# Kernel tuning notes

Hardware: AMD Instinct MI355X
Metric: run time of the kernel (lower is better)

Reference implementation:

```python
import jax, jax.numpy as jnp
import numpy as np
from jax import lax

# Dims from LSTMTagger class constants
B, S, LP = 1024, 128, 14       # sentences, words/sentence, padded chars/word
K, CE, WE, Lf = 3, 6, 10, 4    # char window, char emb, word emb, cnn filters
H, V, A, T = 6, 50000, 100, 135  # lstm hidden, vocab, alphabet, tagset
D = WE + Lf                     # lstm input dim = 14
LW = LP - K + 1                 # conv windows per word = 12


def setup_inputs() -> dict:
    key = jax.random.key(0)
    ks = jax.random.split(key, 14)
    n = lambda k, shp: jax.random.normal(k, shp, dtype=jnp.float32) * 0.1
    inp = {
        "word_idx": jax.random.randint(ks[0], (B, S), 0, V, dtype=jnp.int32),
        "char_idx": jax.random.randint(ks[1], (B, S, LP), 0, A, dtype=jnp.int32),
        "word_emb": n(ks[2], (V, WE)),
        "char_emb": n(ks[3], (A, CE)),
        "Wc": n(ks[4], (Lf, K * CE)),   # Conv1d(1, l, K*CE) weight, squeezed
        "bc": n(ks[5], (Lf,)),
        "Wih_f": n(ks[6], (4 * H, D)),
        "Whh_f": n(ks[7], (4 * H, H)),
        "b_f": n(ks[8], (4 * H,)),      # b_ih + b_hh fused (equivalent)
        "Wih_b": n(ks[9], (4 * H, D)),
        "Whh_b": n(ks[10], (4 * H, H)),
        "b_b": n(ks[11], (4 * H,)),
        "Wt": n(ks[12], (T, 2 * H)),
        "bt": n(ks[13], (T,)),
    }
    return inp


def _lstm_scan(xs, Wih, Whh, b):
    # xs: [S, B, D] -> hs: [S, B, H]; torch gate order i, f, g, o
    h0 = jnp.zeros((xs.shape[1], H), xs.dtype)

    def step(carry, xt):
        h, c = carry
        g = xt @ Wih.T + h @ Whh.T + b
        i, f, gg, o = jnp.split(g, 4, axis=-1)
        c = jax.nn.sigmoid(f) * c + jax.nn.sigmoid(i) * jnp.tanh(gg)
        h = jax.nn.sigmoid(o) * jnp.tanh(c)
        return (h, c), h

    _, hs = lax.scan(step, (h0, h0), xs)
    return hs


def reference(word_emb, char_emb, Wc, bc, Wih_f, Whh_f, b_f,
              Wih_b, Whh_b, b_b, Wt, bt, word_idx, char_idx):
    # per-word char CNN: sliding K-char windows, flatten, linear, max-pool
    ce = char_emb[char_idx]                              # [B,S,LP,CE]
    windows = jnp.concatenate([ce[:, :, i:i + LW] for i in range(K)], axis=-1)  # [B,S,LW,K*CE]
    phi = jnp.einsum('bswk,lk->bswl', windows, Wc) + bc  # [B,S,LW,Lf]
    char_repr = phi.max(axis=2)                          # [B,S,Lf]

    we = word_emb[word_idx]                              # [B,S,WE]
    x = jnp.concatenate([we, char_repr], axis=-1)        # [B,S,D]

    xs = x.transpose(1, 0, 2)                            # [S,B,D]
    hf = _lstm_scan(xs, Wih_f, Whh_f, b_f)               # forward direction
    hb = _lstm_scan(xs[::-1], Wih_b, Whh_b, b_b)[::-1]   # backward direction
    out = jnp.concatenate([hf, hb], axis=-1).transpose(1, 0, 2)  # [B,S,2H]

    tag_space = out @ Wt.T + bt                          # [B,S,T]
    return jax.nn.log_softmax(tag_space, axis=-1)
```

## Files before the change

### kernel.cpp

```cpp
#include <hip/hip_runtime.h>

#define B_   1024
#define S_   128
#define LP_  14
#define K_   3
#define CE_  6
#define WE_  10
#define LF_  4
#define H_   6
#define D_   14
#define T_   135
#define LW_  12
#define V_   50000
#define A_   100
#define NSEQ (B_ * 2)

static __device__ __forceinline__ float fsigm(float x) {
    return __frcp_rn(1.0f + __expf(-x));
}
static __device__ __forceinline__ float ftanh(float x) {
    return fmaf(2.0f, __frcp_rn(1.0f + __expf(-2.0f * x)), -1.0f);
}

static __device__ __forceinline__ float wave_sum64(float s) {
    int v = __float_as_int(s);
    float f;
    f = __int_as_float(__builtin_amdgcn_update_dpp(0, v, 0xB1, 0xF, 0xF, true));  s += f; v = __float_as_int(s);
    f = __int_as_float(__builtin_amdgcn_update_dpp(0, v, 0x4E, 0xF, 0xF, true));  s += f; v = __float_as_int(s);
    f = __int_as_float(__builtin_amdgcn_update_dpp(0, v, 0x141, 0xF, 0xF, true)); s += f; v = __float_as_int(s);
    f = __int_as_float(__builtin_amdgcn_update_dpp(0, v, 0x140, 0xF, 0xF, true)); s += f; v = __float_as_int(s);
    f = __int_as_float(__builtin_amdgcn_update_dpp(0, v, 0x142, 0xA, 0xF, true)); s += f; v = __float_as_int(s);
    f = __int_as_float(__builtin_amdgcn_update_dpp(0, v, 0x143, 0xC, 0xF, true)); s += f; v = __float_as_int(s);
    return __int_as_float(__builtin_amdgcn_readlane(v, 63));
}

__global__ __launch_bounds__(256) void k_e(
    const int* __restrict__ word_idx, const int* __restrict__ char_idx,
    const float* __restrict__ word_emb, const float* __restrict__ char_emb,
    const float* __restrict__ Wc, const float* __restrict__ bc,
    const float* __restrict__ Wih_f, const float* __restrict__ b_f,
    const float* __restrict__ Wih_b, const float* __restrict__ b_b,
    float* __restrict__ gbuf)
{
    __shared__ float s_ce[A_ * CE_];
    __shared__ float s_wc[LF_ * K_ * CE_];
    __shared__ float s_bc[LF_];
    int t = threadIdx.x;
    for (int e = t; e < A_ * CE_; e += 256) s_ce[e] = char_emb[e];
    if (t < LF_ * K_ * CE_) s_wc[t] = Wc[t];
    if (t < LF_) s_bc[t] = bc[t];
    __syncthreads();

    int wid = blockIdx.x * 256 + t;
    int s = wid >> 10;
    int b = wid & 1023;
    int w = b * S_ + s;

    const int2* ci2 = (const int2*)(char_idx + (size_t)w * LP_);
    int idxs[LP_];
    #pragma unroll
    for (int p = 0; p < 7; ++p) {
        int2 v = ci2[p];
        idxs[2 * p] = v.x; idxs[2 * p + 1] = v.y;
    }
    float ce[LP_][CE_];
    #pragma unroll
    for (int p = 0; p < LP_; ++p) {
        int idx = idxs[p];
        idx = idx < 0 ? 0 : (idx >= A_ ? A_ - 1 : idx);
        #pragma unroll
        for (int c = 0; c < CE_; ++c) ce[p][c] = s_ce[idx * CE_ + c];
    }
    float x[D_];
    #pragma unroll
    for (int l = 0; l < LF_; ++l) {
        float acc[LW_];
        float bl = s_bc[l];
        #pragma unroll
        for (int q = 0; q < LW_; ++q) acc[q] = bl;
        #pragma unroll
        for (int kk = 0; kk < K_; ++kk) {
            #pragma unroll
            for (int c = 0; c < CE_; ++c) {
                float wv_ = s_wc[l * (K_ * CE_) + kk * CE_ + c];
                #pragma unroll
                for (int q = 0; q < LW_; ++q) acc[q] = fmaf(ce[q + kk][c], wv_, acc[q]);
            }
        }
        float m = acc[0];
        #pragma unroll
        for (int q = 1; q < LW_; ++q) m = fmaxf(m, acc[q]);
        x[WE_ + l] = m;
    }
    int wi = word_idx[w];
    wi = wi < 0 ? 0 : (wi >= V_ ? V_ - 1 : wi);
    const float2* wep = (const float2*)(word_emb + (size_t)wi * WE_);
    #pragma unroll
    for (int c = 0; c < WE_ / 2; ++c) {
        float2 v = wep[c];
        x[2 * c] = v.x; x[2 * c + 1] = v.y;
    }

    float* dst = gbuf + ((size_t)s * NSEQ + 2 * b) * 24;
    {
        float g[24];
        #pragma unroll
        for (int r = 0; r < 24; ++r) {
            float a = b_f[r];
            #pragma unroll
            for (int k = 0; k < D_; ++k) a = fmaf(Wih_f[r * D_ + k], x[k], a);
            g[r] = a;
        }
        #pragma unroll
        for (int u = 0; u < H_; ++u)
            ((float4*)dst)[u] = make_float4(g[u], g[H_ + u], g[2 * H_ + u], g[3 * H_ + u]);
    }
    {
        float g[24];
        #pragma unroll
        for (int r = 0; r < 24; ++r) {
            float a = b_b[r];
            #pragma unroll
            for (int k = 0; k < D_; ++k) a = fmaf(Wih_b[r * D_ + k], x[k], a);
            g[r] = a;
        }
        #pragma unroll
        for (int u = 0; u < H_; ++u)
            ((float4*)(dst + 24))[u] = make_float4(g[u], g[H_ + u], g[2 * H_ + u], g[3 * H_ + u]);
    }
}

__global__ __launch_bounds__(64) void k_l(
    const float* __restrict__ Whh_f, const float* __restrict__ Whh_b,
    const float* __restrict__ gbuf, float* __restrict__ hbuf)
{
    int lane = threadIdx.x;
    int grp  = lane >> 3;
    int u8   = lane & 7;
    bool act = (u8 < H_);
    int u    = act ? u8 : (H_ - 1);
    int seq  = blockIdx.x * 8 + grp;
    int b    = seq >> 1;
    int dir  = seq & 1;
    int gb   = grp << 3;

    const float* Whh = dir ? Whh_b : Whh_f;
    float w0[H_], w1[H_], w2[H_], w3[H_];
    #pragma unroll
    for (int k = 0; k < H_; ++k) {
        w0[k] = Whh[(0 * H_ + u) * H_ + k];
        w1[k] = Whh[(1 * H_ + u) * H_ + k];
        w2[k] = Whh[(2 * H_ + u) * H_ + k];
        w3[k] = Whh[(3 * H_ + u) * H_ + k];
    }

    const long gstride = (dir ? -1L : 1L) * (long)(NSEQ * 24);
    const float* gp = gbuf + ((size_t)(dir ? S_ - 1 : 0) * NSEQ + (size_t)seq) * 24 + u * 4;

    float4 pf[8];
    #pragma unroll
    for (int j = 0; j < 8; ++j) pf[j] = *(const float4*)(gp + j * gstride);
    const float* gn = gp + 8 * gstride;

    float* hp = hbuf + ((size_t)b * S_ + (size_t)(dir ? S_ - 1 : 0)) * 12 + dir * H_ + u;
    const int hstride = dir ? -12 : 12;

    float h[H_];
    #pragma unroll
    for (int k = 0; k < H_; ++k) h[k] = 0.f;
    float c = 0.f;

    for (int m = 0; m < S_; m += 8) {
        #pragma unroll
        for (int j = 0; j < 8; ++j) {
            float4 g4 = pf[j];
            if (m + 8 + j < S_) {
                pf[j] = *(const float4*)gn;
                gn += gstride;
            }
            float ai = g4.x, af = g4.y, ag = g4.z, ao = g4.w;
            #pragma unroll
            for (int k = 0; k < H_; ++k) {
                ai = fmaf(w0[k], h[k], ai);
                af = fmaf(w1[k], h[k], af);
                ag = fmaf(w2[k], h[k], ag);
                ao = fmaf(w3[k], h[k], ao);
            }
            float si = fsigm(ai), sf = fsigm(af), so = fsigm(ao), tg = ftanh(ag);
            c = fmaf(sf, c, si * tg);
            float hu = so * ftanh(c);
            if (act) *hp = hu;
            hp += hstride;
            #pragma unroll
            for (int k = 0; k < H_; ++k) h[k] = __shfl(hu, gb + k, 64);
        }
    }
}

__global__ __launch_bounds__(256) void k_p(
    const float* __restrict__ hbuf,
    const float* __restrict__ Wt, const float* __restrict__ bt,
    float* __restrict__ out)
{
    __shared__ float s_hb[64 * 12];
    int t = threadIdx.x;
    int ib = blockIdx.x * 64;
    {
        const float4* src = (const float4*)(hbuf + (size_t)ib * 12);
        float4* dst = (float4*)s_hb;
        if (t < 192) dst[t] = src[t];
    }
    __syncthreads();

    int lane = t & 63, wv = t >> 6;
    bool has2 = (lane < T_ - 128);
    int t2c = has2 ? (lane + 128) : (T_ - 1);

    float wA[12], wB[12], wC[12];
    #pragma unroll
    for (int jj = 0; jj < 12; ++jj) {
        wA[jj] = Wt[lane * 12 + jj];
        wB[jj] = Wt[(lane + 64) * 12 + jj];
        wC[jj] = Wt[t2c * 12 + jj];
    }
    float bA = bt[lane], bB = bt[lane + 64], bC = bt[t2c];

    int it0 = wv * 16;
    #pragma unroll 4
    for (int k = 0; k < 16; ++k) {
        int it = it0 + k;
        const float4* h4 = (const float4*)(s_hb + it * 12);
        float4 a0 = h4[0], a1 = h4[1], a2 = h4[2];
        float hv[12] = {a0.x, a0.y, a0.z, a0.w, a1.x, a1.y, a1.z, a1.w, a2.x, a2.y, a2.z, a2.w};
        float y0 = bA, y1 = bB, y2 = bC;
        #pragma unroll
        for (int jj = 0; jj < 12; ++jj) {
            y0 = fmaf(hv[jj], wA[jj], y0);
            y1 = fmaf(hv[jj], wB[jj], y1);
            y2 = fmaf(hv[jj], wC[jj], y2);
        }
        float ss = __expf(y0) + __expf(y1) + (has2 ? __expf(y2) : 0.0f);
        float ls = __logf(wave_sum64(ss));
        float* op = out + (size_t)(ib + it) * T_;
        op[lane]      = y0 - ls;
        op[lane + 64] = y1 - ls;
        if (has2) op[lane + 128] = y2 - ls;
    }
}

extern "C" void kernel_launch(void* const* d_in, const int* in_sizes, int n_in,
                              void* d_out, int out_size, void* d_ws, size_t ws_size,
                              hipStream_t stream)
{
    const int* word_idx = (const int*)d_in[0];
    const int* char_idx = (const int*)d_in[1];
    const float* word_emb = (const float*)d_in[2];
    const float* char_emb = (const float*)d_in[3];
    const float* Wc    = (const float*)d_in[4];
    const float* bc    = (const float*)d_in[5];
    const float* Wih_f = (const float*)d_in[6];
    const float* Whh_f = (const float*)d_in[7];
    const float* b_f   = (const float*)d_in[8];
    const float* Wih_b = (const float*)d_in[9];
    const float* Whh_b = (const float*)d_in[10];
    const float* b_b   = (const float*)d_in[11];
    const float* Wt    = (const float*)d_in[12];
    const float* bt    = (const float*)d_in[13];

    const size_t hbuf_fl = (size_t)B_ * S_ * 12;
    const size_t gbuf_fl = (size_t)S_ * NSEQ * 24;

    float* hbuf = (float*)d_ws;
    float* gbuf;
    if (ws_size >= (hbuf_fl + gbuf_fl) * sizeof(float)) {
        gbuf = (float*)d_ws + hbuf_fl;
    } else {
        gbuf = (float*)d_out;
    }

    k_e<<<(B_ * S_) / 256, 256, 0, stream>>>(word_idx, char_idx, word_emb, char_emb,
                                             Wc, bc, Wih_f, b_f, Wih_b, b_b, gbuf);
    k_l<<<NSEQ / 8, 64, 0, stream>>>(Whh_f, Whh_b, gbuf, hbuf);
    k_p<<<(B_ * S_) / 64, 256, 0, stream>>>(hbuf, Wt, bt, (float*)d_out);
}
```

Baseline: 181.9 us.

## Map one batch element per wave and broadcast hidden state via readlane

Reassigns the recurrent LSTM kernel so each 64-lane wave handles one batch element's forward and backward sequences in its two halves, launching one block per batch element. Hidden-state broadcast uses scalar readlane instead of cross-lane shuffles, and each gate dot product is split into two partial sums to shorten the dependency chain. The goal is lower per-timestep latency on the serial recurrence and more waves in flight, at the cost of many idle lanes per wave.

After: 186.1 us. 2.3% more time.

```diff
diff --git a/kernel.cpp b/kernel.cpp
--- a/kernel.cpp
+++ b/kernel.cpp
@@ -135,14 +135,12 @@
     const float* __restrict__ gbuf, float* __restrict__ hbuf)
 {
     int lane = threadIdx.x;
-    int grp  = lane >> 3;
-    int u8   = lane & 7;
-    bool act = (u8 < H_);
-    int u    = act ? u8 : (H_ - 1);
-    int seq  = blockIdx.x * 8 + grp;
-    int b    = seq >> 1;
-    int dir  = seq & 1;
-    int gb   = grp << 3;
+    int dir  = lane >> 5;
+    int u32  = lane & 31;
+    bool act = (u32 < H_);
+    int u    = act ? u32 : (H_ - 1);
+    int b    = blockIdx.x;
+    int seq  = 2 * b + dir;
 
     const float* Whh = dir ? Whh_b : Whh_f;
     float w0[H_], w1[H_], w2[H_], w3[H_];
@@ -178,21 +176,28 @@
                 pf[j] = *(const float4*)gn;
                 gn += gstride;
             }
-            float ai = g4.x, af = g4.y, ag = g4.z, ao = g4.w;
-            #pragma unroll
-            for (int k = 0; k < H_; ++k) {
-                ai = fmaf(w0[k], h[k], ai);
-                af = fmaf(w1[k], h[k], af);
-                ag = fmaf(w2[k], h[k], ag);
-                ao = fmaf(w3[k], h[k], ao);
-            }
-            float si = fsigm(ai), sf = fsigm(af), so = fsigm(ao), tg = ftanh(ag);
+            float ai0 = fmaf(w0[0], h[0], g4.x); ai0 = fmaf(w0[1], h[1], ai0); ai0 = fmaf(w0[2], h[2], ai0);
+            float ai1 =      w0[3] * h[3];       ai1 = fmaf(w0[4], h[4], ai1); ai1 = fmaf(w0[5], h[5], ai1);
+            float af0 = fmaf(w1[0], h[0], g4.y); af0 = fmaf(w1[1], h[1], af0); af0 = fmaf(w1[2], h[2], af0);
+            float af1 =      w1[3] * h[3];       af1 = fmaf(w1[4], h[4], af1); af1 = fmaf(w1[5], h[5], af1);
+            float ag0 = fmaf(w2[0], h[0], g4.z); ag0 = fmaf(w2[1], h[1], ag0); ag0 = fmaf(w2[2], h[2], ag0);
+            float ag1 =      w2[3] * h[3];       ag1 = fmaf(w2[4], h[4], ag1); ag1 = fmaf(w2[5], h[5], ag1);
+            float ao0 = fmaf(w3[0], h[0], g4.w); ao0 = fmaf(w3[1], h[1], ao0); ao0 = fmaf(w3[2], h[2], ao0);
+            float ao1 =      w3[3] * h[3];       ao1 = fmaf(w3[4], h[4], ao1); ao1 = fmaf(w3[5], h[5], ao1);
+            float si = fsigm(ai0 + ai1);
+            float sf = fsigm(af0 + af1);
+            float so = fsigm(ao0 + ao1);
+            float tg = ftanh(ag0 + ag1);
             c = fmaf(sf, c, si * tg);
             float hu = so * ftanh(c);
             if (act) *hp = hu;
             hp += hstride;
             #pragma unroll
-            for (int k = 0; k < H_; ++k) h[k] = __shfl(hu, gb + k, 64);
+            for (int k = 0; k < H_; ++k) {
+                int vf = __builtin_amdgcn_readlane(__float_as_int(hu), k);
+                int vb = __builtin_amdgcn_readlane(__float_as_int(hu), 32 + k);
+                h[k] = __int_as_float(dir ? vb : vf);
+            }
         }
     }
 }
@@ -280,6 +285,6 @@
 
     k_e<<<(B_ * S_) / 256, 256, 0, stream>>>(word_idx, char_idx, word_emb, char_emb,
                                              Wc, bc, Wih_f, b_f, Wih_b, b_b, gbuf);
-    k_l<<<NSEQ / 8, 64, 0, stream>>>(Whh_f, Whh_b, gbuf, hbuf);
+    k_l<<<B_, 64, 0, stream>>>(Whh_f, Whh_b, gbuf, hbuf);
     k_p<<<(B_ * S_) / 64, 256, 0, stream>>>(hbuf, Wt, bt, (float*)d_out);
 }
```

## Remap LSTM recurrence to one batch per wave with readlane broadcast and padded prefetch

Applied to the files above, without the earlier changes.

Each 64-lane wave now handles one batch element, with the forward direction in the low 32 lanes and the backward direction in the high 32, instead of packing eight sequences per wave. That quadruples the number of waves available to hide the serial recurrence latency. The hidden-state broadcast now uses scalar readlane instead of the __shfl (ds_bpermute) cross-lane path. The gate buffer is padded by PADR rows at both ends so the deeper 16-step prefetch can read unconditionally without a bounds branch. In exchange, most lanes do redundant work and there are more waves, registers and memory for the padded buffer.

Measured after the change: 178.9 us. No clear change (-1.6%).

```diff
diff --git a/kernel.cpp b/kernel.cpp
--- a/kernel.cpp
+++ b/kernel.cpp
@@ -14,6 +14,7 @@
 #define V_   50000
 #define A_   100
 #define NSEQ (B_ * 2)
+#define PADR 16
 
 static __device__ __forceinline__ float fsigm(float x) {
     return __frcp_rn(1.0f + __expf(-x));
@@ -135,14 +136,11 @@
     const float* __restrict__ gbuf, float* __restrict__ hbuf)
 {
     int lane = threadIdx.x;
-    int grp  = lane >> 3;
-    int u8   = lane & 7;
-    bool act = (u8 < H_);
-    int u    = act ? u8 : (H_ - 1);
-    int seq  = blockIdx.x * 8 + grp;
-    int b    = seq >> 1;
-    int dir  = seq & 1;
-    int gb   = grp << 3;
+    int dir  = lane >> 5;
+    int u32  = lane & 31;
+    int u    = (u32 < H_) ? u32 : (H_ - 1);
+    int b    = blockIdx.x;
+    int seq  = 2 * b + dir;
 
     const float* Whh = dir ? Whh_b : Whh_f;
     float w0[H_], w1[H_], w2[H_], w3[H_];
@@ -157,10 +155,10 @@
     const long gstride = (dir ? -1L : 1L) * (long)(NSEQ * 24);
     const float* gp = gbuf + ((size_t)(dir ? S_ - 1 : 0) * NSEQ + (size_t)seq) * 24 + u * 4;
 
-    float4 pf[8];
-    #pragma unroll
-    for (int j = 0; j < 8; ++j) pf[j] = *(const float4*)(gp + j * gstride);
-    const float* gn = gp + 8 * gstride;
+    float4 pf[PADR];
+    #pragma unroll
+    for (int j = 0; j < PADR; ++j) pf[j] = *(const float4*)(gp + j * gstride);
+    const float* gn = gp + PADR * gstride;
 
     float* hp = hbuf + ((size_t)b * S_ + (size_t)(dir ? S_ - 1 : 0)) * 12 + dir * H_ + u;
     const int hstride = dir ? -12 : 12;
@@ -170,14 +168,14 @@
     for (int k = 0; k < H_; ++k) h[k] = 0.f;
     float c = 0.f;
 
-    for (int m = 0; m < S_; m += 8) {
-        #pragma unroll
-        for (int j = 0; j < 8; ++j) {
+    #pragma unroll 1
+    for (int m = 0; m < S_; m += PADR) {
+        #pragma unroll
+        for (int j = 0; j < PADR; ++j) {
             float4 g4 = pf[j];
-            if (m + 8 + j < S_) {
-                pf[j] = *(const float4*)gn;
-                gn += gstride;
-            }
+            pf[j] = *(const float4*)gn;
+            gn += gstride;
+
             float ai = g4.x, af = g4.y, ag = g4.z, ao = g4.w;
             #pragma unroll
             for (int k = 0; k < H_; ++k) {
@@ -189,10 +187,16 @@
             float si = fsigm(ai), sf = fsigm(af), so = fsigm(ao), tg = ftanh(ag);
             c = fmaf(sf, c, si * tg);
             float hu = so * ftanh(c);
-            if (act) *hp = hu;
+
+            *hp = hu;
             hp += hstride;
-            #pragma unroll
-            for (int k = 0; k < H_; ++k) h[k] = __shfl(hu, gb + k, 64);
+
+            #pragma unroll
+            for (int k = 0; k < H_; ++k) {
+                int vf = __builtin_amdgcn_readlane(__float_as_int(hu), k);
+                int vb = __builtin_amdgcn_readlane(__float_as_int(hu), 32 + k);
+                h[k] = __int_as_float(dir ? vb : vf);
+            }
         }
     }
 }
@@ -268,18 +272,20 @@
     const float* bt    = (const float*)d_in[13];
 
     const size_t hbuf_fl = (size_t)B_ * S_ * 12;
-    const size_t gbuf_fl = (size_t)S_ * NSEQ * 24;
+    const size_t grow_fl = (size_t)NSEQ * 24;
+    const size_t galloc_fl = (size_t)(S_ + 2 * PADR) * grow_fl;
 
     float* hbuf = (float*)d_ws;
-    float* gbuf;
-    if (ws_size >= (hbuf_fl + gbuf_fl) * sizeof(float)) {
-        gbuf = (float*)d_ws + hbuf_fl;
+    float* galloc;
+    if (ws_size >= (hbuf_fl + galloc_fl) * sizeof(float)) {
+        galloc = (float*)d_ws + hbuf_fl;
     } else {
-        gbuf = (float*)d_out;
-    }
+        galloc = (float*)d_out;
+    }
+    float* gbuf = galloc + PADR * grow_fl;
 
     k_e<<<(B_ * S_) / 256, 256, 0, stream>>>(word_idx, char_idx, word_emb, char_emb,
                                              Wc, bc, Wih_f, b_f, Wih_b, b_b, gbuf);
-    k_l<<<NSEQ / 8, 64, 0, stream>>>(Whh_f, Whh_b, gbuf, hbuf);
+    k_l<<<B_, 64, 0, stream>>>(Whh_f, Whh_b, gbuf, hbuf);
     k_p<<<(B_ * S_) / 64, 256, 0, stream>>>(hbuf, Wt, bt, (float*)d_out);
 }
```

## Fuse char-CNN embedding and bidirectional LSTM into one per-sentence kernel via LDS

Applied to the files above, without the earlier changes.

Merges the embedding/input-projection kernel with the LSTM recurrence kernel. Each 128-thread block now handles one sentence: the threads compute the gate pre-activations for all words into shared memory, then one wave runs the forward scan and the other runs the backward scan. Hidden states are exchanged with readlane instead of shuffles and written to shared memory before one coalesced store. This removes the large global gate buffer round trip and one launch. The trade-off is that only 6 lanes per wave do useful work in the serial scan, where before 8 sequences were packed into each wave.

Measured after the change: 188.6 us. +3.7%, slower.

```diff
diff --git a/kernel.cpp b/kernel.cpp
--- a/kernel.cpp
+++ b/kernel.cpp
@@ -13,7 +13,7 @@
 #define LW_  12
 #define V_   50000
 #define A_   100
-#define NSEQ (B_ * 2)
+#define SGST 52
 
 static __device__ __forceinline__ float fsigm(float x) {
     return __frcp_rn(1.0f + __expf(-x));
@@ -34,166 +34,169 @@
     return __int_as_float(__builtin_amdgcn_readlane(v, 63));
 }
 
-__global__ __launch_bounds__(256) void k_e(
+__global__ __launch_bounds__(128, 2) void k_f(
     const int* __restrict__ word_idx, const int* __restrict__ char_idx,
     const float* __restrict__ word_emb, const float* __restrict__ char_emb,
     const float* __restrict__ Wc, const float* __restrict__ bc,
-    const float* __restrict__ Wih_f, const float* __restrict__ b_f,
-    const float* __restrict__ Wih_b, const float* __restrict__ b_b,
-    float* __restrict__ gbuf)
+    const float* __restrict__ Wih_f, const float* __restrict__ Whh_f, const float* __restrict__ b_f,
+    const float* __restrict__ Wih_b, const float* __restrict__ Whh_b, const float* __restrict__ b_b,
+    float* __restrict__ hbuf)
 {
+    __shared__ __align__(16) float s_g[S_][SGST];
+    __shared__ __align__(16) float s_h[S_][12];
     __shared__ float s_ce[A_ * CE_];
     __shared__ float s_wc[LF_ * K_ * CE_];
     __shared__ float s_bc[LF_];
+
     int t = threadIdx.x;
-    for (int e = t; e < A_ * CE_; e += 256) s_ce[e] = char_emb[e];
+    int b = blockIdx.x;
+
+    for (int e = t; e < A_ * CE_; e += 128) s_ce[e] = char_emb[e];
     if (t < LF_ * K_ * CE_) s_wc[t] = Wc[t];
     if (t < LF_) s_bc[t] = bc[t];
     __syncthreads();
 
-    int wid = blockIdx.x * 256 + t;
-    int s = wid >> 10;
-    int b = wid & 1023;
-    int w = b * S_ + s;
-
-    const int2* ci2 = (const int2*)(char_idx + (size_t)w * LP_);
-    int idxs[LP_];
-    #pragma unroll
-    for (int p = 0; p < 7; ++p) {
-        int2 v = ci2[p];
-        idxs[2 * p] = v.x; idxs[2 * p + 1] = v.y;
-    }
-    float ce[LP_][CE_];
-    #pragma unroll
-    for (int p = 0; p < LP_; ++p) {
-        int idx = idxs[p];
-        idx = idx < 0 ? 0 : (idx >= A_ ? A_ - 1 : idx);
-        #pragma unroll
-        for (int c = 0; c < CE_; ++c) ce[p][c] = s_ce[idx * CE_ + c];
-    }
-    float x[D_];
-    #pragma unroll
-    for (int l = 0; l < LF_; ++l) {
-        float acc[LW_];
-        float bl = s_bc[l];
-        #pragma unroll
-        for (int q = 0; q < LW_; ++q) acc[q] = bl;
-        #pragma unroll
-        for (int kk = 0; kk < K_; ++kk) {
-            #pragma unroll
-            for (int c = 0; c < CE_; ++c) {
-                float wv_ = s_wc[l * (K_ * CE_) + kk * CE_ + c];
+    {
+        int w = b * S_ + t;
+        const int2* ci2 = (const int2*)(char_idx + (size_t)w * LP_);
+        int idxs[LP_];
+        #pragma unroll
+        for (int p = 0; p < 7; ++p) {
+            int2 v = ci2[p];
+            idxs[2 * p] = v.x; idxs[2 * p + 1] = v.y;
+        }
+        float ce[LP_][CE_];
+        #pragma unroll
+        for (int p = 0; p < LP_; ++p) {
+            int idx = idxs[p];
+            idx = idx < 0 ? 0 : (idx >= A_ ? A_ - 1 : idx);
+            #pragma unroll
+            for (int c = 0; c < CE_; ++c) ce[p][c] = s_ce[idx * CE_ + c];
+        }
+        float x[D_];
+        #pragma unroll
+        for (int l = 0; l < LF_; ++l) {
+            float acc[LW_];
+            float bl = s_bc[l];
+            #pragma unroll
+            for (int q = 0; q < LW_; ++q) acc[q] = bl;
+            #pragma unroll
+            for (int kk = 0; kk < K_; ++kk) {
                 #pragma unroll
-                for (int q = 0; q < LW_; ++q) acc[q] = fmaf(ce[q + kk][c], wv_, acc[q]);
+                for (int c = 0; c < CE_; ++c) {
+                    float wv_ = s_wc[l * (K_ * CE_) + kk * CE_ + c];
+                    #pragma unroll
+                    for (int q = 0; q < LW_; ++q) acc[q] = fmaf(ce[q + kk][c], wv_, acc[q]);
+                }
             }
-        }
-        float m = acc[0];
-        #pragma unroll
-        for (int q = 1; q < LW_; ++q) m = fmaxf(m, acc[q]);
-        x[WE_ + l] = m;
-    }
-    int wi = word_idx[w];
-    wi = wi < 0 ? 0 : (wi >= V_ ? V_ - 1 : wi);
-    const float2* wep = (const float2*)(word_emb + (size_t)wi * WE_);
-    #pragma unroll
-    for (int c = 0; c < WE_ / 2; ++c) {
-        float2 v = wep[c];
-        x[2 * c] = v.x; x[2 * c + 1] = v.y;
-    }
-
-    float* dst = gbuf + ((size_t)s * NSEQ + 2 * b) * 24;
-    {
-        float g[24];
-        #pragma unroll
-        for (int r = 0; r < 24; ++r) {
-            float a = b_f[r];
-            #pragma unroll
-            for (int k = 0; k < D_; ++k) a = fmaf(Wih_f[r * D_ + k], x[k], a);
-            g[r] = a;
-        }
-        #pragma unroll
-        for (int u = 0; u < H_; ++u)
-            ((float4*)dst)[u] = make_float4(g[u], g[H_ + u], g[2 * H_ + u], g[3 * H_ + u]);
-    }
-    {
-        float g[24];
-        #pragma unroll
-        for (int r = 0; r < 24; ++r) {
-            float a = b_b[r];
-            #pragma unroll
-            for (int k = 0; k < D_; ++k) a = fmaf(Wih_b[r * D_ + k], x[k], a);
-            g[r] = a;
-        }
-        #pragma unroll
-        for (int u = 0; u < H_; ++u)
-            ((float4*)(dst + 24))[u] = make_float4(g[u], g[H_ + u], g[2 * H_ + u], g[3 * H_ + u]);
-    }
-}
-
-__global__ __launch_bounds__(64) void k_l(
-    const float* __restrict__ Whh_f, const float* __restrict__ Whh_b,
-    const float* __restrict__ gbuf, float* __restrict__ hbuf)
-{
-    int lane = threadIdx.x;
-    int grp  = lane >> 3;
-    int u8   = lane & 7;
-    bool act = (u8 < H_);
-    int u    = act ? u8 : (H_ - 1);
-    int seq  = blockIdx.x * 8 + grp;
-    int b    = seq >> 1;
-    int dir  = seq & 1;
-    int gb   = grp << 3;
-
-    const float* Whh = dir ? Whh_b : Whh_f;
-    float w0[H_], w1[H_], w2[H_], w3[H_];
-    #pragma unroll
-    for (int k = 0; k < H_; ++k) {
-        w0[k] = Whh[(0 * H_ + u) * H_ + k];
-        w1[k] = Whh[(1 * H_ + u) * H_ + k];
-        w2[k] = Whh[(2 * H_ + u) * H_ + k];
-        w3[k] = Whh[(3 * H_ + u) * H_ + k];
-    }
-
-    const long gstride = (dir ? -1L : 1L) * (long)(NSEQ * 24);
-    const float* gp = gbuf + ((size_t)(dir ? S_ - 1 : 0) * NSEQ + (size_t)seq) * 24 + u * 4;
-
-    float4 pf[8];
-    #pragma unroll
-    for (int j = 0; j < 8; ++j) pf[j] = *(const float4*)(gp + j * gstride);
-    const float* gn = gp + 8 * gstride;
-
-    float* hp = hbuf + ((size_t)b * S_ + (size_t)(dir ? S_ - 1 : 0)) * 12 + dir * H_ + u;
-    const int hstride = dir ? -12 : 12;
-
-    float h[H_];
-    #pragma unroll
-    for (int k = 0; k < H_; ++k) h[k] = 0.f;
-    float c = 0.f;
-
-    for (int m = 0; m < S_; m += 8) {
-        #pragma unroll
-        for (int j = 0; j < 8; ++j) {
-            float4 g4 = pf[j];
-            if (m + 8 + j < S_) {
-                pf[j] = *(const float4*)gn;
-                gn += gstride;
+            float m = acc[0];
+            #pragma unroll
+            for (int q = 1; q < LW_; ++q) m = fmaxf(m, acc[q]);
+            x[WE_ + l] = m;
+        }
+        int wi = word_idx[w];
+        wi = wi < 0 ? 0 : (wi >= V_ ? V_ - 1 : wi);
+        const float2* wep = (const float2*)(word_emb + (size_t)wi * WE_);
+        #pragma unroll
+        for (int c = 0; c < WE_ / 2; ++c) {
+            float2 v = wep[c];
+            x[2 * c] = v.x; x[2 * c + 1] = v.y;
+        }
+
+        float4* dstf = (float4*)&s_g[t][0];
+        {
+            float g[24];
+            #pragma unroll
+            for (int r = 0; r < 24; ++r) {
+                float a = b_f[r];
+                #pragma unroll
+                for (int k = 0; k < D_; ++k) a = fmaf(Wih_f[r * D_ + k], x[k], a);
+                g[r] = a;
             }
-            float ai = g4.x, af = g4.y, ag = g4.z, ao = g4.w;
-            #pragma unroll
-            for (int k = 0; k < H_; ++k) {
-                ai = fmaf(w0[k], h[k], ai);
-                af = fmaf(w1[k], h[k], af);
-                ag = fmaf(w2[k], h[k], ag);
-                ao = fmaf(w3[k], h[k], ao);
+            #pragma unroll
+            for (int u = 0; u < H_; ++u)
+                dstf[u] = make_float4(g[u], g[H_ + u], g[2 * H_ + u], g[3 * H_ + u]);
+        }
+        float4* dstb = (float4*)&s_g[t][24];
+        {
+            float g[24];
+            #pragma unroll
+            for (int r = 0; r < 24; ++r) {
+                float a = b_b[r];
+                #pragma unroll
+                for (int k = 0; k < D_; ++k) a = fmaf(Wih_b[r * D_ + k], x[k], a);
+                g[r] = a;
             }
-            float si = fsigm(ai), sf = fsigm(af), so = fsigm(ao), tg = ftanh(ag);
-            c = fmaf(sf, c, si * tg);
-            float hu = so * ftanh(c);
-            if (act) *hp = hu;
-            hp += hstride;
-            #pragma unroll
-            for (int k = 0; k < H_; ++k) h[k] = __shfl(hu, gb + k, 64);
-        }
+            #pragma unroll
+            for (int u = 0; u < H_; ++u)
+                dstb[u] = make_float4(g[u], g[H_ + u], g[2 * H_ + u], g[3 * H_ + u]);
+        }
+    }
+    __syncthreads();
+
+    {
+        int wv   = t >> 6;
+        int lane = t & 63;
+        bool act = (lane < H_);
+        int u    = act ? lane : (H_ - 1);
+
+        const float* Whh = wv ? Whh_b : Whh_f;
+        float w0[H_], w1[H_], w2[H_], w3[H_];
+        #pragma unroll
+        for (int k = 0; k < H_; ++k) {
+            w0[k] = Whh[(0 * H_ + u) * H_ + k];
+            w1[k] = Whh[(1 * H_ + u) * H_ + k];
+            w2[k] = Whh[(2 * H_ + u) * H_ + k];
+            w3[k] = Whh[(3 * H_ + u) * H_ + k];
+        }
+
+        const float* gp = &s_g[wv ? (S_ - 1) : 0][wv * 24 + u * 4];
+        const int gstep = wv ? -SGST : SGST;
+
+        float h[H_];
+        #pragma unroll
+        for (int k = 0; k < H_; ++k) h[k] = 0.f;
+        float c = 0.f;
+
+        float4 g4 = *(const float4*)gp;
+
+#define LSTEP(G4, J)                                                            \
+        {                                                                       \
+            float ai = (G4).x, af = (G4).y, ag = (G4).z, ao = (G4).w;           \
+            _Pragma("unroll")                                                   \
+            for (int k = 0; k < H_; ++k) {                                      \
+                ai = fmaf(w0[k], h[k], ai);                                     \
+                af = fmaf(w1[k], h[k], af);                                     \
+                ag = fmaf(w2[k], h[k], ag);                                     \
+                ao = fmaf(w3[k], h[k], ao);                                     \
+            }                                                                   \
+            float si = fsigm(ai), sf = fsigm(af), so = fsigm(ao), tg = ftanh(ag); \
+            c = fmaf(sf, c, si * tg);                                           \
+            float hu = so * ftanh(c);                                           \
+            int se = wv ? (S_ - 1 - (J)) : (J);                                 \
+            if (act) s_h[se][wv * H_ + u] = hu;                                 \
+            _Pragma("unroll")                                                   \
+            for (int k = 0; k < H_; ++k)                                        \
+                h[k] = __int_as_float(__builtin_amdgcn_readlane(__float_as_int(hu), k)); \
+        }
+
+        #pragma unroll 4
+        for (int j = 0; j < S_ - 1; ++j) {
+            gp += gstep;
+            float4 nx = *(const float4*)gp;
+            LSTEP(g4, j);
+            g4 = nx;
+        }
+        LSTEP(g4, S_ - 1);
+#undef LSTEP
+    }
+    __syncthreads();
+
+    {
+        float4* dst = (float4*)(hbuf + (size_t)b * S_ * 12);
+        const float4* src = (const float4*)&s_h[0][0];
+        #pragma unroll
+        for (int i = 0; i < 3; ++i) dst[t + 128 * i] = src[t + 128 * i];
     }
 }
 
@@ -267,19 +270,9 @@
     const float* Wt    = (const float*)d_in[12];
     const float* bt    = (const float*)d_in[13];
 
-    const size_t hbuf_fl = (size_t)B_ * S_ * 12;
-    const size_t gbuf_fl = (size_t)S_ * NSEQ * 24;
-
     float* hbuf = (float*)d_ws;
-    float* gbuf;
-    if (ws_size >= (hbuf_fl + gbuf_fl) * sizeof(float)) {
-        gbuf = (float*)d_ws + hbuf_fl;
-    } else {
-        gbuf = (float*)d_out;
-    }
-
-    k_e<<<(B_ * S_) / 256, 256, 0, stream>>>(word_idx, char_idx, word_emb, char_emb,
-                                             Wc, bc, Wih_f, b_f, Wih_b, b_b, gbuf);
-    k_l<<<NSEQ / 8, 64, 0, stream>>>(Whh_f, Whh_b, gbuf, hbuf);
+
+    k_f<<<B_, 128, 0, stream>>>(word_idx, char_idx, word_emb, char_emb, Wc, bc,
+                                Wih_f, Whh_f, b_f, Wih_b, Whh_b, b_b, hbuf);
     k_p<<<(B_ * S_) / 64, 256, 0, stream>>>(hbuf, Wt, bt, (float*)d_out);
 }
```
